# Optimization experiments

Measured on AMD Instinct MI355X. Metric: run time of the kernel, lower is better.

Reference implementation:

```python
import jax, jax.numpy as jnp
import numpy as np

N, M, E, D = 100000, 20000, 1600000, 128


def setup_inputs() -> dict:
    key = jax.random.key(0)
    ks = jax.random.split(key, 14)
    s = 1.0 / np.sqrt(D)
    inp = {
        "x": jax.random.normal(ks[0], (N, D), jnp.float32),
        "in_src": jax.random.randint(ks[1], (E,), 0, N),
        "in_dst": jax.random.randint(ks[2], (E,), 0, M),
        "has_src": jax.random.randint(ks[3], (E,), 0, M),
        "has_dst": jax.random.randint(ks[4], (E,), 0, N),
        "W1": jax.random.normal(ks[5], (D, D), jnp.float32) * s,
        "b1": jnp.zeros((D,), jnp.float32),
        "an1": jax.random.normal(ks[6], (D, 1), jnp.float32) * s,
        "ae1": jax.random.normal(ks[7], (D, 1), jnp.float32) * s,
        "W2": jax.random.normal(ks[8], (D, D), jnp.float32) * s,
        "b2": jnp.zeros((D,), jnp.float32),
        "an2": jax.random.normal(ks[9], (D, 1), jnp.float32) * s,
        "ae2": jax.random.normal(ks[10], (D, 1), jnp.float32) * s,
    }
    return inp


def _hgat_layer(x, W, b, an, ae, in_src, in_dst, has_src, has_dst, activate):
    h = x @ W + b                       # [N, D] fc transform
    n_attn = h @ an                     # [N, 1] node attn scores
    # node -> hyperedge ('in' edges). h_e is unset at this point (local_scope),
    # so the hyperedge bias term is zero; e = attn[src].
    e = n_attn[in_src]                  # [E, 1]
    # source uses F.softmax(e, dim=0): GLOBAL softmax over all edges
    attn = jax.nn.softmax(e, axis=0)    # [E, 1]
    h_e = jax.ops.segment_sum(attn * h[in_src], in_dst, num_segments=M)  # [M, D]
    e_attn = h_e @ ae                   # [M, 1] hyperedge attn scores
    # hyperedge -> node ('has' edges): bias is node attn score at dst
    e2 = e_attn[has_src] + n_attn[has_dst]  # [E, 1]
    attn2 = jax.nn.softmax(e2, axis=0)      # global softmax over all edges
    h_n = jax.ops.segment_sum(attn2 * h_e[has_src], has_dst, num_segments=N)  # [N, D]
    return jax.nn.relu(h_n) if activate else h_n


def reference(x, in_src, in_dst, has_src, has_dst,
              W1, b1, an1, ae1, W2, b2, an2, ae2):
    # layer 1 (activation=relu), layer 2 (no activation); dropout in eval mode
    h = _hgat_layer(x, W1, b1, an1, ae1, in_src, in_dst, has_src, has_dst, True)
    h = _hgat_layer(h, W2, b2, an2, ae2, in_src, in_dst, has_src, has_dst, False)
    return h
```

## Files before the change

### kernel.cpp

```cpp
#include <hip/hip_runtime.h>
#include <hip/hip_bf16.h>
#include <math.h>
#include <type_traits>


typedef unsigned int u32;
typedef unsigned short u16;
typedef u16 u16x8 __attribute__((ext_vector_type(8)));
typedef short bf16x8 __attribute__((ext_vector_type(8)));
typedef float f32x4 __attribute__((ext_vector_type(4)));

#define NCONST 100000
#define MCONST 20000
#define ECONST 1600000
#define HCH2 32768
#define HBC 32

#define PBLK 256
#define PT 6250
#define SHB_IN 6
#define NBK_IN 313
#define SRCB_IN 17
#define SHB_HAS 8
#define NBK_HAS 391
#define SRCB_HAS 15

__device__ __forceinline__ u16 f2bf(float f) {
  u32 u = __float_as_uint(f);
  u += 0x7FFFu + ((u >> 16) & 1u);
  return (u16)(u >> 16);
}
__device__ __forceinline__ float bf2f(u16 b) {
  return __uint_as_float(((u32)b) << 16);
}

__global__ __launch_bounds__(256) void k_hpart2(const int* __restrict__ in_dst,
                                                const int* __restrict__ has_dst,
                                                const int* __restrict__ in_src,
                                                int* __restrict__ partial) {
  __shared__ int hc[HCH2];
  int y = blockIdx.y;
  const int* __restrict__ arr = (y == 0) ? in_dst : (y <= 4 ? has_dst : in_src);
  int lo = (y == 0) ? 0 : (y <= 4 ? (y - 1) * HCH2 : (y - 5) * HCH2);
  for (int i = threadIdx.x; i < HCH2; i += 256) hc[i] = 0;
  __syncthreads();
  int stride = gridDim.x * 256;
  int n4 = ECONST >> 2;
  const int4* a4 = (const int4*)arr;
  for (int i = blockIdx.x * 256 + threadIdx.x; i < n4; i += stride) {
    int4 v = a4[i];
    u32 a = (u32)(v.x - lo), b = (u32)(v.y - lo), c = (u32)(v.z - lo), d = (u32)(v.w - lo);
    if (a < HCH2) atomicAdd(&hc[a], 1);
    if (b < HCH2) atomicAdd(&hc[b], 1);
    if (c < HCH2) atomicAdd(&hc[c], 1);
    if (d < HCH2) atomicAdd(&hc[d], 1);
  }
  __syncthreads();
  int* out = partial + ((size_t)y * HBC + blockIdx.x) * HCH2;
  for (int i = threadIdx.x; i < HCH2; i += 256) out[i] = hc[i];
}

__global__ void k_scan1d(const int* __restrict__ partial, int nM, int nN,
                         int* __restrict__ off_in, int* __restrict__ off_has,
                         int* __restrict__ deg, int* __restrict__ bsum) {
  __shared__ int sd[256];
  int y = blockIdx.y;
  int n = y ? nN : nM;
  int rowbase = (y == 0) ? 0 : (y == 1 ? 1 : 5);
  int t = threadIdx.x;
  int base = blockIdx.x * 1024 + t * 4;
  int v[4];
#pragma unroll
  for (int k = 0; k < 4; ++k) {
    int j = base + k;
    int s = 0;
    if (j < n) {
      int chunk = j >> 15;
      int jl = j & (HCH2 - 1);
      const int* p = partial + ((size_t)(rowbase + chunk) * HBC) * HCH2 + jl;
#pragma unroll
      for (int b = 0; b < HBC; ++b) s += p[(size_t)b * HCH2];
    }
    v[k] = s;
  }
  if (y == 2) {
#pragma unroll
    for (int k = 0; k < 4; ++k)
      if (base + k < n) deg[base + k] = v[k];
    return;
  }
  int* off = y ? off_has : off_in;
  int* bs = bsum + y * 128;
  v[1] += v[0]; v[2] += v[1]; v[3] += v[2];
  int tot = v[3];
  sd[t] = tot;
  __syncthreads();
  for (int o = 1; o < 256; o <<= 1) {
    int x = (t >= o) ? sd[t - o] : 0;
    __syncthreads();
    sd[t] += x;
    __syncthreads();
  }
  int excl = sd[t] - tot;
#pragma unroll
  for (int k = 0; k < 4; ++k)
    if (base + k < n) off[base + k + 1] = v[k] + excl;
  if (t == 255) bs[blockIdx.x] = sd[255];
}

__global__ void k_scan2d(int* __restrict__ bsum, int nbM, int nbN) {
  __shared__ int sd[256];
  int* bs = bsum + blockIdx.x * 128;
  int nb = blockIdx.x ? nbN : nbM;
  int t = threadIdx.x;
  int v = (t < nb) ? bs[t] : 0;
  sd[t] = v;
  __syncthreads();
  for (int o = 1; o < 256; o <<= 1) {
    int x = (t >= o) ? sd[t - o] : 0;
    __syncthreads();
    sd[t] += x;
    __syncthreads();
  }
  if (t < nb) bs[t] = sd[t] - v;
}

__global__ void k_scan3d(int* __restrict__ off_in, int* __restrict__ off_has,
                         const int* __restrict__ bsum, int nM, int nN) {
  int y = blockIdx.y;
  int* off = y ? off_has : off_in;
  const int* bs = bsum + y * 128;
  int n = y ? nN : nM;
  int i = blockIdx.x * blockDim.x + threadIdx.x;
  int st = gridDim.x * blockDim.x;
  if (blockIdx.x == 0 && threadIdx.x == 0) off[0] = 0;
  for (; i < n; i += st) off[i + 1] += bs[i >> 10];
}

__global__ __launch_bounds__(256) void k_coarse(const int* __restrict__ in_dst,
                                                const int* __restrict__ has_dst,
                                                int* __restrict__ bb_in,
                                                int* __restrict__ bb_has) {
  __shared__ int h1[NBK_IN];
  __shared__ int h2[NBK_HAS];
  for (int i = threadIdx.x; i < NBK_IN; i += 256) h1[i] = 0;
  for (int i = threadIdx.x; i < NBK_HAS; i += 256) h2[i] = 0;
  __syncthreads();
  int c0 = blockIdx.x * PT, c1 = min(c0 + PT, ECONST);
  for (int i = c0 + threadIdx.x; i < c1; i += 256) {
    atomicAdd(&h1[in_dst[i] >> SHB_IN], 1);
    atomicAdd(&h2[has_dst[i] >> SHB_HAS], 1);
  }
  __syncthreads();
  int* o1 = bb_in + (size_t)blockIdx.x * NBK_IN;
  for (int i = threadIdx.x; i < NBK_IN; i += 256) o1[i] = h1[i];
  int* o2 = bb_has + (size_t)blockIdx.x * NBK_HAS;
  for (int i = threadIdx.x; i < NBK_HAS; i += 256) o2[i] = h2[i];
}

template <int NBUK, int SHB>
__device__ __forceinline__ void colscan_body(int* __restrict__ bb,
                                             const int* __restrict__ off, int segs,
                                             int* sd) {
  int b = blockIdx.x;
  if (b >= NBUK) return;
  int t = threadIdx.x;
  int v = bb[(size_t)t * NBUK + b];
  sd[t] = v;
  __syncthreads();
  for (int o = 1; o < 256; o <<= 1) {
    int x = (t >= o) ? sd[t - o] : 0;
    __syncthreads();
    sd[t] += x;
    __syncthreads();
  }
  bb[(size_t)t * NBUK + b] = sd[t] - v + off[min(b << SHB, segs)];
}

__global__ __launch_bounds__(256) void k_colscan2(int* __restrict__ bb_in,
                                                  const int* __restrict__ off_in,
                                                  int* __restrict__ bb_has,
                                                  const int* __restrict__ off_has) {
  __shared__ int sd[256];
  if (blockIdx.y == 0)
    colscan_body<NBK_IN, SHB_IN>(bb_in, off_in, MCONST, sd);
  else
    colscan_body<NBK_HAS, SHB_HAS>(bb_has, off_has, NCONST, sd);
}

template <int NBUK, int SHB, int SRCB>
__device__ __forceinline__ void stage_body(const int* __restrict__ dst,
                                           const int* __restrict__ srcv,
                                           const int* __restrict__ bb,
                                           int* __restrict__ ebuf, int* hist, int* loff,
                                           int* gbase, int* stg, int* sd) {
  int t = threadIdx.x;
  for (int i = t; i < NBUK; i += 256) hist[i] = 0;
  __syncthreads();
  int c0 = blockIdx.x * PT, c1 = min(c0 + PT, ECONST);
  for (int i = c0 + t; i < c1; i += 256) atomicAdd(&hist[dst[i] >> SHB], 1);
  __syncthreads();
  {
    int v0 = (2 * t < NBUK) ? hist[2 * t] : 0;
    int v1 = (2 * t + 1 < NBUK) ? hist[2 * t + 1] : 0;
    sd[t] = v0 + v1;
    __syncthreads();
    for (int o = 1; o < 256; o <<= 1) {
      int x = (t >= o) ? sd[t - o] : 0;
      __syncthreads();
      sd[t] += x;
      __syncthreads();
    }
    int excl = sd[t] - (v0 + v1);
    if (2 * t < NBUK) loff[2 * t] = excl;
    if (2 * t + 1 < NBUK) loff[2 * t + 1] = excl + v0;
  }
  __syncthreads();
  for (int i = t; i < NBUK; i += 256) {
    gbase[i] = bb[(size_t)blockIdx.x * NBUK + i];
    hist[i] = loff[i];
  }
  __syncthreads();
  for (int i = c0 + t; i < c1; i += 256) {
    int d = dst[i], s = srcv[i];
    int b = d >> SHB;
    int r = atomicAdd(&hist[b], 1);
    stg[r] = (b << 23) | ((d & ((1 << SHB) - 1)) << SRCB) | s;
  }
  __syncthreads();
  int tot = c1 - c0;
  for (int i = t; i < tot; i += 256) {
    int v = stg[i];
    int b = ((u32)v) >> 23;
    ebuf[gbase[b] + (i - loff[b])] = v & ((1 << 23) - 1);
  }
}

__global__ __launch_bounds__(256) void k_stage2(
    const int* __restrict__ in_dst, const int* __restrict__ in_src,
    const int* __restrict__ bb_in, int* __restrict__ ebuf_in,
    const int* __restrict__ has_dst, const int* __restrict__ has_src,
    const int* __restrict__ bb_has, int* __restrict__ ebuf_has) {
  __shared__ int hist[NBK_HAS];
  __shared__ int loff[NBK_HAS];
  __shared__ int gbase[NBK_HAS];
  __shared__ int stg[PT];
  __shared__ int sd[256];
  if (blockIdx.y == 0)
    stage_body<NBK_IN, SHB_IN, SRCB_IN>(in_dst, in_src, bb_in, ebuf_in, hist, loff, gbase,
                                        stg, sd);
  else
    stage_body<NBK_HAS, SHB_HAS, SRCB_HAS>(has_dst, has_src, bb_has, ebuf_has, hist, loff,
                                           gbase, stg, sd);
}

template <int SHB, int SRCB>
__device__ __forceinline__ void place_body(const int* __restrict__ off, int segs,
                                           const int* __restrict__ ebuf,
                                           int* __restrict__ csrc, int* cur) {
  const int NSEG = 1 << SHB;
  int seg0 = blockIdx.x << SHB;
  if (seg0 >= segs) return;
  int segN = min(seg0 + NSEG, segs);
  for (int i = threadIdx.x; i < segN - seg0; i += 256) cur[i] = off[seg0 + i];
  __syncthreads();
  int start = off[seg0], end = off[segN];
  for (int i = start + threadIdx.x; i < end; i += 256) {
    int v = ebuf[i];
    int dloc = ((u32)v) >> SRCB;
    int pos = atomicAdd(&cur[dloc], 1);
    csrc[pos] = v & ((1 << SRCB) - 1);
  }
}

__global__ __launch_bounds__(256) void k_place2(
    const int* __restrict__ off_in, const int* __restrict__ ebuf_in,
    int* __restrict__ csrc_in, const int* __restrict__ off_has,
    const int* __restrict__ ebuf_has, int* __restrict__ csrc_has) {
  __shared__ int cur[256];
  if (blockIdx.y == 0)
    place_body<SHB_IN, SRCB_IN>(off_in, MCONST, ebuf_in, csrc_in, cur);
  else
    place_body<SHB_HAS, SRCB_HAS>(off_has, NCONST, ebuf_has, csrc_has, cur);
}

__device__ __forceinline__ void merge_write(float m, float s, float2* __restrict__ pairs) {
  for (int o = 1; o < 64; o <<= 1) {
    float om = __shfl_xor(m, o, 64), os = __shfl_xor(s, o, 64);
    float nm = fmaxf(m, om);
    s = s * __expf(m - nm) + os * __expf(om - nm);
    m = nm;
  }
  __shared__ float sm[4], ss[4];
  int t = threadIdx.x;
  if ((t & 63) == 0) { sm[t >> 6] = m; ss[t >> 6] = s; }
  __syncthreads();
  if (t == 0) {
    for (int k = 1; k < 4; ++k) {
      float nm = fmaxf(m, sm[k]);
      s = s * __expf(m - nm) + ss[k] * __expf(sm[k] - nm);
      m = nm;
    }
    pairs[blockIdx.x] = make_float2(m, s);
  }
}

template <typename IT>
__global__ __launch_bounds__(256, 3) void k_fc(
    const IT* __restrict__ x, const float* __restrict__ W,
    const float* __restrict__ bias, const float* __restrict__ an,
    const int* __restrict__ deg, u16* __restrict__ h, float* __restrict__ na,
    float2* __restrict__ pairs, int nrows) {
  __shared__ __align__(16) u16 sWT[128 * 136];
  __shared__ float sNa[128];
  int tid = threadIdx.x;
  int lane = tid & 63, w = tid >> 6;
  int cl = lane & 15, qg = lane >> 4;

  for (int i = tid * 4; i < 16384; i += 1024) {
    float4 v = *(const float4*)(W + i);
    int k = i >> 7, j = i & 127;
    sWT[(j + 0) * 136 + k] = f2bf(v.x);
    sWT[(j + 1) * 136 + k] = f2bf(v.y);
    sWT[(j + 2) * 136 + k] = f2bf(v.z);
    sWT[(j + 3) * 136 + k] = f2bf(v.w);
  }

  float anv[8], bv[8];
#pragma unroll
  for (int t = 0; t < 8; ++t) {
    anv[t] = an[t * 16 + cl];
    bv[t] = bias[t * 16 + cl];
  }

  int rbase = blockIdx.x * 128 + w * 32;
  bf16x8 afr[2][4];
#pragma unroll
  for (int g = 0; g < 2; ++g) {
    int r = rbase + g * 16 + cl;
    int rc = min(r, nrows - 1);
    const IT* xp = x + (size_t)rc * 128 + qg * 8;
#pragma unroll
    for (int s = 0; s < 4; ++s) {
      if constexpr (sizeof(IT) == 4) {
        float4 u0 = *(const float4*)(xp + s * 32);
        float4 u1 = *(const float4*)(xp + s * 32 + 4);
        bf16x8 a;
        a[0] = (short)f2bf(u0.x); a[1] = (short)f2bf(u0.y);
        a[2] = (short)f2bf(u0.z); a[3] = (short)f2bf(u0.w);
        a[4] = (short)f2bf(u1.x); a[5] = (short)f2bf(u1.y);
        a[6] = (short)f2bf(u1.z); a[7] = (short)f2bf(u1.w);
        afr[g][s] = a;
      } else {
        afr[g][s] = *(const bf16x8*)(xp + s * 32);
      }
    }
  }
  __syncthreads();

  f32x4 acc[2][8];
#pragma unroll
  for (int g = 0; g < 2; ++g)
#pragma unroll
    for (int t = 0; t < 8; ++t) {
      acc[g][t][0] = 0.f; acc[g][t][1] = 0.f; acc[g][t][2] = 0.f; acc[g][t][3] = 0.f;
    }

#pragma unroll
  for (int t = 0; t < 8; ++t) {
    bf16x8 bfrg[4];
    const u16* bp = sWT + (t * 16 + cl) * 136 + qg * 8;
#pragma unroll
    for (int s = 0; s < 4; ++s) bfrg[s] = *(const bf16x8*)(bp + s * 32);
#pragma unroll
    for (int s = 0; s < 4; ++s) {
#pragma unroll
      for (int g = 0; g < 2; ++g)
        acc[g][t] = __builtin_amdgcn_mfma_f32_16x16x32_bf16(afr[g][s], bfrg[s], acc[g][t],
                                                            0, 0, 0);
    }
  }

  float pa[2][4];
#pragma unroll
  for (int g = 0; g < 2; ++g)
#pragma unroll
    for (int reg = 0; reg < 4; ++reg) pa[g][reg] = 0.f;
#pragma unroll
  for (int g = 0; g < 2; ++g)
#pragma unroll
    for (int t = 0; t < 8; ++t)
#pragma unroll
      for (int reg = 0; reg < 4; ++reg)
        pa[g][reg] = fmaf(acc[g][t][reg] + bv[t], anv[t], pa[g][reg]);
#pragma unroll
  for (int g = 0; g < 2; ++g)
#pragma unroll
    for (int reg = 0; reg < 4; ++reg) {
      float v = pa[g][reg];
      v += __shfl_xor(v, 1, 64);
      v += __shfl_xor(v, 2, 64);
      v += __shfl_xor(v, 4, 64);
      v += __shfl_xor(v, 8, 64);
      pa[g][reg] = v;
    }
  if (cl == 0) {
#pragma unroll
    for (int g = 0; g < 2; ++g)
#pragma unroll
      for (int reg = 0; reg < 4; ++reg) {
        int r = rbase + g * 16 + qg * 4 + reg;
        int lidx = w * 32 + g * 16 + qg * 4 + reg;
        if (r < nrows) {
          na[r] = pa[g][reg];
          sNa[lidx] = pa[g][reg];
        }
      }
  }

  __syncthreads();
  u16* st = sWT + w * 32 * 136;
#pragma unroll
  for (int g = 0; g < 2; ++g)
#pragma unroll
    for (int t = 0; t < 8; ++t)
#pragma unroll
      for (int reg = 0; reg < 4; ++reg)
        st[(g * 16 + qg * 4 + reg) * 136 + t * 16 + cl] = f2bf(acc[g][t][reg] + bv[t]);
#pragma unroll
  for (int it = 0; it < 8; ++it) {
    int idx = it * 64 + lane;
    int row = idx >> 4, c = idx & 15;
    u16x8 v = *(const u16x8*)(st + row * 136 + c * 8);
    int r = rbase + row;
    if (r < nrows) *(u16x8*)(h + (size_t)r * 128 + c * 8) = v;
  }

  float m1 = -1e30f, s1 = 0.f;
  if (tid < 128) {
    int r = blockIdx.x * 128 + tid;
    if (r < nrows) {
      int d = deg[r];
      if (d > 0) { m1 = sNa[tid]; s1 = (float)d; }
    }
  }
  merge_write(m1, s1, pairs);
}

__global__ void k_sm2(const float* __restrict__ ea, const float* __restrict__ na,
                      const int* __restrict__ hs, const int* __restrict__ hd, int n,
                      float2* __restrict__ pairs) {
  float m = -1e30f, s = 0.f;
  int i = blockIdx.x * blockDim.x + threadIdx.x;
  int st = gridDim.x * blockDim.x;
  for (; i < n; i += st) {
    float xv = ea[hs[i]] + na[hd[i]];
    if (xv > m) { s *= __expf(m - xv); m = xv; }
    s += __expf(xv - m);
  }
  merge_write(m, s, pairs);
}

__global__ void k_smfin(const float2* __restrict__ pairs, int nb, float* __restrict__ out) {
  int t = threadIdx.x;
  float m = -1e30f, s = 0.f;
  for (int i = t; i < nb; i += 256) {
    float2 pr = pairs[i];
    float nm = fmaxf(m, pr.x);
    s = s * __expf(m - nm) + pr.y * __expf(pr.x - nm);
    m = nm;
  }
  for (int o = 1; o < 64; o <<= 1) {
    float om = __shfl_xor(m, o, 64), os = __shfl_xor(s, o, 64);
    float nm = fmaxf(m, om);
    s = s * __expf(m - nm) + os * __expf(om - nm);
    m = nm;
  }
  __shared__ float sm[4], ss[4];
  if ((t & 63) == 0) { sm[t >> 6] = m; ss[t >> 6] = s; }
  __syncthreads();
  if (t == 0) {
    for (int k = 1; k < 4; ++k) {
      float nm = fmaxf(m, sm[k]);
      s = s * __expf(m - nm) + ss[k] * __expf(sm[k] - nm);
      m = nm;
    }
    out[0] = m;
    out[1] = s;
  }
}

__global__ __launch_bounds__(256) void k_segA(
    const u16* __restrict__ h, const float* __restrict__ na,
    const float* __restrict__ scal, const int* __restrict__ csrc,
    const int* __restrict__ off, const float* __restrict__ ae, u16* __restrict__ he,
    float* __restrict__ ea, int m_count) {
  int wid = (blockIdx.x << 2) + (threadIdx.x >> 6);
  if (wid >= m_count) return;
  float mx = scal[0];
  float iz = 1.0f / scal[1];
  int lane = threadIdx.x & 63;
  int eslot = lane >> 3, cl = lane & 7;
  int s = off[wid], t = off[wid + 1];
  float ax[16];
#pragma unroll
  for (int j = 0; j < 16; ++j) ax[j] = 0.f;
  for (int i = s + eslot; i < t; i += 8) {
    int sr = csrc[i];
    float ww = __expf(na[sr] - mx) * iz;
    const u16* hp = h + (size_t)sr * 128 + cl * 16;
    u16x8 v0 = *(const u16x8*)(hp);
    u16x8 v1 = *(const u16x8*)(hp + 8);
#pragma unroll
    for (int j = 0; j < 8; ++j) {
      ax[j] = fmaf(ww, bf2f(v0[j]), ax[j]);
      ax[8 + j] = fmaf(ww, bf2f(v1[j]), ax[8 + j]);
    }
  }
#pragma unroll
  for (int j = 0; j < 16; ++j) {
    ax[j] += __shfl_xor(ax[j], 8, 64);
    ax[j] += __shfl_xor(ax[j], 16, 64);
    ax[j] += __shfl_xor(ax[j], 32, 64);
  }
  const float* aep = ae + cl * 16;
  float pa = 0.f;
#pragma unroll
  for (int j = 0; j < 16; ++j) pa = fmaf(ax[j], aep[j], pa);
  pa += __shfl_xor(pa, 1, 64);
  pa += __shfl_xor(pa, 2, 64);
  pa += __shfl_xor(pa, 4, 64);
  if (eslot == 0) {
    u16x8 o0, o1;
#pragma unroll
    for (int j = 0; j < 8; ++j) { o0[j] = f2bf(ax[j]); o1[j] = f2bf(ax[8 + j]); }
    u16* hep = he + (size_t)wid * 128 + cl * 16;
    *(u16x8*)(hep) = o0;
    *(u16x8*)(hep + 8) = o1;
    if (cl == 0) ea[wid] = pa;
  }
}

template <int L1>
__global__ __launch_bounds__(256) void k_segB(
    const u16* __restrict__ he, const float* __restrict__ ea,
    const float* __restrict__ na, const float* __restrict__ scal,
    const int* __restrict__ csrc, const int* __restrict__ off,
    void* __restrict__ yout, int n_count) {
  int wid = (blockIdx.x << 2) + (threadIdx.x >> 6);
  if (wid >= n_count) return;
  float mx2 = scal[2];
  float iz2 = 1.0f / scal[3];
  int lane = threadIdx.x & 63;
  int eslot = lane >> 3, cl = lane & 7;
  float nav = na[wid];
  int s = off[wid], t = off[wid + 1];
  float ax[16];
#pragma unroll
  for (int j = 0; j < 16; ++j) ax[j] = 0.f;
  for (int i = s + eslot; i < t; i += 8) {
    int sr = csrc[i];
    float c = __expf(ea[sr] + nav - mx2) * iz2;
    const u16* hp = he + (size_t)sr * 128 + cl * 16;
    u16x8 v0 = *(const u16x8*)(hp);
    u16x8 v1 = *(const u16x8*)(hp + 8);
#pragma unroll
    for (int j = 0; j < 8; ++j) {
      ax[j] = fmaf(c, bf2f(v0[j]), ax[j]);
      ax[8 + j] = fmaf(c, bf2f(v1[j]), ax[8 + j]);
    }
  }
#pragma unroll
  for (int j = 0; j < 16; ++j) {
    ax[j] += __shfl_xor(ax[j], 8, 64);
    ax[j] += __shfl_xor(ax[j], 16, 64);
    ax[j] += __shfl_xor(ax[j], 32, 64);
    if (L1) ax[j] = fmaxf(ax[j], 0.f);
  }
  if (eslot == 0) {
    if (L1) {
      u16x8 o0, o1;
#pragma unroll
      for (int j = 0; j < 8; ++j) { o0[j] = f2bf(ax[j]); o1[j] = f2bf(ax[8 + j]); }
      u16* yp = (u16*)yout + (size_t)wid * 128 + cl * 16;
      *(u16x8*)(yp) = o0;
      *(u16x8*)(yp + 8) = o1;
    } else {
      float* y = (float*)yout + (size_t)wid * 128 + cl * 16;
      *(float4*)(y + 0) = make_float4(ax[0], ax[1], ax[2], ax[3]);
      *(float4*)(y + 4) = make_float4(ax[4], ax[5], ax[6], ax[7]);
      *(float4*)(y + 8) = make_float4(ax[8], ax[9], ax[10], ax[11]);
      *(float4*)(y + 12) = make_float4(ax[12], ax[13], ax[14], ax[15]);
    }
  }
}

extern "C" void kernel_launch(void* const* d_in, const int* in_sizes, int n_in,
                              void* d_out, int out_size, void* d_ws, size_t ws_size,
                              hipStream_t stream) {
  const int N = NCONST, M = MCONST, E = ECONST;
  const float* x = (const float*)d_in[0];
  const int* in_src = (const int*)d_in[1];
  const int* in_dst = (const int*)d_in[2];
  const int* has_src = (const int*)d_in[3];
  const int* has_dst = (const int*)d_in[4];
  const float* W1 = (const float*)d_in[5];
  const float* b1 = (const float*)d_in[6];
  const float* an1 = (const float*)d_in[7];
  const float* ae1 = (const float*)d_in[8];
  const float* W2 = (const float*)d_in[9];
  const float* b2 = (const float*)d_in[10];
  const float* an2 = (const float*)d_in[11];
  const float* ae2 = (const float*)d_in[12];

  const size_t PARTIAL_BYTES = (size_t)9 * HBC * HCH2 * 4;

  char* p = (char*)d_ws;
  auto alloc = [&](size_t bytes) {
    char* q = p;
    p += (bytes + 255) & ~(size_t)255;
    return q;
  };
  u16* h = (u16*)alloc((size_t)N * 128 * 2);
  u16* he = (u16*)alloc((size_t)M * 128 * 2);
  float* na = (float*)alloc((size_t)N * 4);
  float* ea = (float*)alloc((size_t)M * 4);
  int* deg = (int*)alloc((size_t)N * 4);
  int* off_in = (int*)alloc((size_t)(M + 1) * 4);
  int* off_has = (int*)alloc((size_t)(N + 1) * 4);
  int* csrc_in = (int*)alloc((size_t)E * 4);
  int* csrc_has = (int*)alloc((size_t)E * 4);
  int* partial = (int*)alloc(PARTIAL_BYTES);
  int* ebuf_in = partial;
  int* ebuf_has = partial + ECONST;
  int* bb_in = (int*)alloc((size_t)PBLK * NBK_IN * 4);
  int* bb_has = (int*)alloc((size_t)PBLK * NBK_HAS * 4);
  int* bsum = (int*)alloc(256 * 4);
  float2* pairs = (float2*)alloc(1024 * 8);
  float* scal = (float*)alloc(64);
  if ((size_t)(p - (char*)d_ws) > ws_size) return;

  u16* y1b = (u16*)d_out;

  k_hpart2<<<dim3(HBC, 9), 256, 0, stream>>>(in_dst, has_dst, in_src, partial);
  int nbM = (M + 1023) / 1024, nbN = (N + 1023) / 1024;
  k_scan1d<<<dim3(nbN, 3), 256, 0, stream>>>(partial, M, N, off_in, off_has, deg, bsum);
  k_scan2d<<<2, 256, 0, stream>>>(bsum, nbM, nbN);
  k_scan3d<<<dim3(512, 2), 256, 0, stream>>>(off_in, off_has, bsum, M, N);

  k_coarse<<<PBLK, 256, 0, stream>>>(in_dst, has_dst, bb_in, bb_has);
  k_colscan2<<<dim3(NBK_HAS, 2), 256, 0, stream>>>(bb_in, off_in, bb_has, off_has);
  k_stage2<<<dim3(PBLK, 2), 256, 0, stream>>>(in_dst, in_src, bb_in, ebuf_in, has_dst,
                                              has_src, bb_has, ebuf_has);
  k_place2<<<dim3(NBK_HAS, 2), 256, 0, stream>>>(off_in, ebuf_in, csrc_in, off_has,
                                                 ebuf_has, csrc_has);

  const int FCB = (N + 127) / 128;
  const int SGB = (M + 3) / 4;
  const int SBB = (N + 3) / 4;

  auto layer = [&](auto xin, const float* W, const float* b, const float* an_,
                   const float* ae_, auto seg_b) {
    using IT = typename std::remove_const<
        typename std::remove_pointer<decltype(xin)>::type>::type;
    k_fc<IT><<<FCB, 256, 0, stream>>>(xin, W, b, an_, deg, h, na, pairs, N);
    k_smfin<<<1, 256, 0, stream>>>(pairs, FCB, scal);
    k_segA<<<SGB, 256, 0, stream>>>(h, na, scal, csrc_in, off_in, ae_, he, ea, M);
    k_sm2<<<256, 256, 0, stream>>>(ea, na, has_src, has_dst, E, pairs);
    k_smfin<<<1, 256, 0, stream>>>(pairs, 256, scal + 2);
    seg_b();
  };

  layer((const float*)x, W1, b1, an1, ae1, [&] {
    k_segB<1><<<SBB, 256, 0, stream>>>(he, ea, na, scal, csrc_has, off_has, (void*)y1b, N);
  });
  layer((const u16*)y1b, W2, b2, an2, ae2, [&] {
    k_segB<0><<<SBB, 256, 0, stream>>>(he, ea, na, scal, csrc_has, off_has, d_out, N);
  });
}
```

Before: 450.9 us.

## Split segB columns across two blocks and precompute per-hyperedge softmax factors

A small kernel now precomputes exp(ea - max)/Z once per hyperedge, so segB does one multiply by exp(na[dst]) per edge instead of an exp. segB is launched with twice as many blocks. Each block handles half of the 128 columns with 16 edge slots of 4 lanes, which adds parallelism and shortens the per-node edge loops. In exchange, the CSR indices and pe values are read twice per node, and exp(na) could overflow for large scores where the old fused exp would not.

```diff
diff --git a/kernel.cpp b/kernel.cpp
--- a/kernel.cpp
+++ b/kernel.cpp
@@ -490,6 +490,13 @@
   }
 }
 
+__global__ __launch_bounds__(256) void k_pe(const float* __restrict__ ea,
+                                            const float* __restrict__ scal,
+                                            float* __restrict__ pe, int m) {
+  int i = blockIdx.x * 256 + threadIdx.x;
+  if (i < m) pe[i] = __expf(ea[i] - scal[2]) * (1.0f / scal[3]);
+}
+
 __global__ __launch_bounds__(256) void k_segA(
     const u16* __restrict__ h, const float* __restrict__ na,
     const float* __restrict__ scal, const int* __restrict__ csrc,
@@ -543,25 +550,25 @@
 
 template <int L1>
 __global__ __launch_bounds__(256) void k_segB(
-    const u16* __restrict__ he, const float* __restrict__ ea,
-    const float* __restrict__ na, const float* __restrict__ scal,
-    const int* __restrict__ csrc, const int* __restrict__ off,
-    void* __restrict__ yout, int n_count) {
-  int wid = (blockIdx.x << 2) + (threadIdx.x >> 6);
+    const u16* __restrict__ he, const float* __restrict__ pe,
+    const float* __restrict__ na, const int* __restrict__ csrc,
+    const int* __restrict__ off, void* __restrict__ yout, int n_count) {
+  int bid = blockIdx.x;
+  int slice = bid & 1;
+  int wid = (bid >> 1) * 4 + (threadIdx.x >> 6);
   if (wid >= n_count) return;
-  float mx2 = scal[2];
-  float iz2 = 1.0f / scal[3];
   int lane = threadIdx.x & 63;
-  int eslot = lane >> 3, cl = lane & 7;
-  float nav = na[wid];
+  int eslot = lane >> 2, cl = lane & 3;
+  float rf = __expf(na[wid]);
   int s = off[wid], t = off[wid + 1];
+  int colb = slice * 64 + cl * 16;
   float ax[16];
 #pragma unroll
   for (int j = 0; j < 16; ++j) ax[j] = 0.f;
-  for (int i = s + eslot; i < t; i += 8) {
+  for (int i = s + eslot; i < t; i += 16) {
     int sr = csrc[i];
-    float c = __expf(ea[sr] + nav - mx2) * iz2;
-    const u16* hp = he + (size_t)sr * 128 + cl * 16;
+    float c = pe[sr] * rf;
+    const u16* hp = he + (size_t)sr * 128 + colb;
     u16x8 v0 = *(const u16x8*)(hp);
     u16x8 v1 = *(const u16x8*)(hp + 8);
 #pragma unroll
@@ -572,6 +579,7 @@
   }
 #pragma unroll
   for (int j = 0; j < 16; ++j) {
+    ax[j] += __shfl_xor(ax[j], 4, 64);
     ax[j] += __shfl_xor(ax[j], 8, 64);
     ax[j] += __shfl_xor(ax[j], 16, 64);
     ax[j] += __shfl_xor(ax[j], 32, 64);
@@ -582,11 +590,11 @@
       u16x8 o0, o1;
 #pragma unroll
       for (int j = 0; j < 8; ++j) { o0[j] = f2bf(ax[j]); o1[j] = f2bf(ax[8 + j]); }
-      u16* yp = (u16*)yout + (size_t)wid * 128 + cl * 16;
+      u16* yp = (u16*)yout + (size_t)wid * 128 + colb;
       *(u16x8*)(yp) = o0;
       *(u16x8*)(yp + 8) = o1;
     } else {
-      float* y = (float*)yout + (size_t)wid * 128 + cl * 16;
+      float* y = (float*)yout + (size_t)wid * 128 + colb;
       *(float4*)(y + 0) = make_float4(ax[0], ax[1], ax[2], ax[3]);
       *(float4*)(y + 4) = make_float4(ax[4], ax[5], ax[6], ax[7]);
       *(float4*)(y + 8) = make_float4(ax[8], ax[9], ax[10], ax[11]);
@@ -625,6 +633,7 @@
   u16* he = (u16*)alloc((size_t)M * 128 * 2);
   float* na = (float*)alloc((size_t)N * 4);
   float* ea = (float*)alloc((size_t)M * 4);
+  float* pe = (float*)alloc((size_t)M * 4);
   int* deg = (int*)alloc((size_t)N * 4);
   int* off_in = (int*)alloc((size_t)(M + 1) * 4);
   int* off_has = (int*)alloc((size_t)(N + 1) * 4);
@@ -657,7 +666,7 @@
 
   const int FCB = (N + 127) / 128;
   const int SGB = (M + 3) / 4;
-  const int SBB = (N + 3) / 4;
+  const int SBB2 = ((N + 3) / 4) * 2;
 
   auto layer = [&](auto xin, const float* W, const float* b, const float* an_,
                    const float* ae_, auto seg_b) {
@@ -668,13 +677,14 @@
     k_segA<<<SGB, 256, 0, stream>>>(h, na, scal, csrc_in, off_in, ae_, he, ea, M);
     k_sm2<<<256, 256, 0, stream>>>(ea, na, has_src, has_dst, E, pairs);
     k_smfin<<<1, 256, 0, stream>>>(pairs, 256, scal + 2);
+    k_pe<<<(M + 255) / 256, 256, 0, stream>>>(ea, scal, pe, M);
     seg_b();
   };
 
   layer((const float*)x, W1, b1, an1, ae1, [&] {
-    k_segB<1><<<SBB, 256, 0, stream>>>(he, ea, na, scal, csrc_has, off_has, (void*)y1b, N);
+    k_segB<1><<<SBB2, 256, 0, stream>>>(he, pe, na, csrc_has, off_has, (void*)y1b, N);
   });
   layer((const u16*)y1b, W2, b2, an2, ae2, [&] {
-    k_segB<0><<<SBB, 256, 0, stream>>>(he, ea, na, scal, csrc_has, off_has, d_out, N);
+    k_segB<0><<<SBB2, 256, 0, stream>>>(he, pe, na, csrc_has, off_has, d_out, N);
   });
 }
```

Result: slower. 609.1 us (+35.1%).
